# Kernel tuning notes

Hardware: AMD Instinct MI355X
Metric: run time of the kernel (lower is better)

Reference implementation:

```python
import jax, jax.numpy as jnp
import numpy as np

N, E, B = 50000, 600000, 64
ANN, D, STEPS, ETYPES, CLS = 64, 128, 5, 4, 10


def setup_inputs() -> dict:
    key = jax.random.key(0)
    ks = jax.random.split(key, 12)
    return {
        "annotation": jax.random.normal(ks[0], (N, ANN), jnp.float32),
        "src": jax.random.randint(ks[1], (E,), 0, N),
        "dst": jax.random.randint(ks[2], (E,), 0, N),
        "etypes": jax.random.randint(ks[3], (E,), 0, ETYPES),
        "node2graph": jnp.sort(jax.random.randint(ks[4], (N,), 0, B)),
        "labels": jax.random.randint(ks[5], (B,), 0, CLS),
        "W_lin": jax.random.normal(ks[6], (ETYPES, D, D), jnp.float32) / np.sqrt(D),
        "b_lin": jnp.zeros((ETYPES, D), jnp.float32),
        "W_ih": jax.random.normal(ks[7], (3 * D, D), jnp.float32) / np.sqrt(D),
        "W_hh": jax.random.normal(ks[8], (3 * D, D), jnp.float32) / np.sqrt(D),
        "b_ih": jnp.zeros((3 * D,), jnp.float32),
        "b_hh": jnp.zeros((3 * D,), jnp.float32),
        "gate_w": jax.random.normal(ks[9], (1, ANN + D), jnp.float32) / np.sqrt(ANN + D),
        "gate_b": jnp.zeros((1,), jnp.float32),
        "out_w": jax.random.normal(ks[10], (CLS, ANN + D), jnp.float32) / np.sqrt(ANN + D),
        "out_b": jnp.zeros((CLS,), jnp.float32),
    }


def reference(annotation, src, dst, etypes, node2graph, labels,
              W_lin, b_lin, W_ih, W_hh, b_ih, b_hh,
              gate_w, gate_b, out_w, out_b):
    n = annotation.shape[0]
    d = W_lin.shape[-1]
    nb = labels.shape[0]
    # h1 = [annotation | zeros]  -> [N, D]
    h = jnp.concatenate(
        [annotation, jnp.zeros((n, d - annotation.shape[1]), annotation.dtype)], -1)

    def step(hc, _):
        # per-edge-type linear transform of all nodes: [K, N, D]
        all_t = jnp.einsum('nd,kod->kno', hc, W_lin) + b_lin[:, None, :]
        m = all_t[etypes, src]                                  # [E, D] messages
        a = jax.ops.segment_sum(m, dst, num_segments=n)         # [N, D] aggregate
        # torch GRUCell: gates ordered (reset, update, new)
        gi = a @ W_ih.T + b_ih
        gh = hc @ W_hh.T + b_hh
        i_r, i_z, i_n = jnp.split(gi, 3, axis=-1)
        h_r, h_z, h_n = jnp.split(gh, 3, axis=-1)
        r = jax.nn.sigmoid(i_r + h_r)
        z = jax.nn.sigmoid(i_z + h_z)
        nt = jnp.tanh(i_n + r * h_n)
        return (1.0 - z) * nt + z * hc, None

    h, _ = jax.lax.scan(step, h, None, length=STEPS)
    feat = jnp.concatenate([h, annotation], -1)                 # [N, D+ANN]
    # global attention pooling: segment softmax over nodes per graph
    gate = (feat @ gate_w.T + gate_b)[:, 0]                     # [N]
    gmax = jax.ops.segment_max(gate, node2graph, num_segments=nb)
    ex = jnp.exp(gate - gmax[node2graph])
    denom = jax.ops.segment_sum(ex, node2graph, num_segments=nb)
    alpha = ex / denom[node2graph]
    readout = jax.ops.segment_sum(feat * alpha[:, None], node2graph, num_segments=nb)
    logits = readout @ out_w.T + out_b                          # [B, CLS]
    preds = jnp.argmax(logits, -1)
    logp = jax.nn.log_softmax(logits, -1)
    loss = -jnp.mean(jnp.take_along_axis(logp, labels[:, None], axis=1))
    return loss, preds
```

## Files before the change

### kernel.cpp

```cpp
#include <hip/hip_runtime.h>
#include <math.h>

#define DD 128
#define ANND 64
#define NSTEPS 5
#define NTYPES 4
#define NCLS 10

typedef __attribute__((ext_vector_type(8))) short short8v;
typedef __attribute__((ext_vector_type(4))) float f32x4;

__device__ __forceinline__ void split2(float x, unsigned short& hi, unsigned short& lo) {
  unsigned u = __float_as_uint(x);
  unsigned hb = (u + 0x7FFFu + ((u >> 16) & 1u)) >> 16;
  hi = (unsigned short)hb;
  float r = x - __uint_as_float(hb << 16);
  unsigned v = __float_as_uint(r);
  lo = (unsigned short)((v + 0x7FFFu + ((v >> 16) & 1u)) >> 16);
}

__device__ __forceinline__ float bf2f(unsigned short u) {
  return __uint_as_float(((unsigned)u) << 16);
}
__device__ __forceinline__ float rec2(const unsigned short* hi, const unsigned short* lo, size_t i) {
  return bf2f(hi[i]) + bf2f(lo[i]);
}
__device__ __forceinline__ float lo16f(unsigned u) { return __uint_as_float(u << 16); }
__device__ __forceinline__ float hi16f(unsigned u) { return __uint_as_float(u & 0xffff0000u); }

__device__ __forceinline__ void gload16(const unsigned short* g, unsigned short* l) {
  __builtin_amdgcn_global_load_lds(
      (const __attribute__((address_space(1))) unsigned int*)(const void*)g,
      (__attribute__((address_space(3))) unsigned int*)(void*)l, 16, 0, 0);
}

__global__ void k_init(const float* __restrict__ ann,
    unsigned short* __restrict__ hhi, unsigned short* __restrict__ hlo, int n, int npad) {
  int idx = blockIdx.x * blockDim.x + threadIdx.x;
  if (idx >= npad * DD) return;
  int node = idx >> 7, d = idx & 127;
  float v = (node < n && d < ANND) ? ann[node * ANND + d] : 0.0f;
  unsigned short hi, lo; split2(v, hi, lo);
  hhi[idx] = hi; hlo[idx] = lo;
}

__global__ void k_deg4(const int* __restrict__ dst, const int* __restrict__ et,
    int* __restrict__ deg4, int e) {
  int i = blockIdx.x * blockDim.x + threadIdx.x;
  if (i < e) atomicAdd(&deg4[dst[i] * 4 + et[i]], 1);
}

__global__ __launch_bounds__(1024) void k_scan(const int* __restrict__ deg4,
    int* __restrict__ base, int n) {
  __shared__ int part[1024];
  int t = threadIdx.x;
  int chunk = (n + 1023) >> 10;
  int s = t * chunk, e = min(n, s + chunk);
  int sum = 0;
  for (int i = s; i < e; ++i) {
    const int4 d4 = *(const int4*)(deg4 + (size_t)i * 4);
    sum += d4.x + d4.y + d4.z + d4.w;
  }
  part[t] = sum;
  __syncthreads();
  int own = sum;
  for (int off = 1; off < 1024; off <<= 1) {
    int v = (t >= off) ? part[t - off] : 0;
    __syncthreads();
    part[t] += v;
    __syncthreads();
  }
  int run = part[t] - own;
  for (int i = s; i < e; ++i) {
    base[i] = run;
    const int4 d4 = *(const int4*)(deg4 + (size_t)i * 4);
    run += d4.x + d4.y + d4.z + d4.w;
  }
  if (s < n && e == n) base[n] = run;
}

__global__ void k_place(const int* __restrict__ src, const int* __restrict__ dst,
    const int* __restrict__ et, const int* __restrict__ base, int* __restrict__ cursor,
    int* __restrict__ cpack, int e) {
  int i = blockIdx.x * blockDim.x + threadIdx.x;
  if (i >= e) return;
  int d = dst[i];
  int pos = base[d] + atomicAdd(&cursor[d], 1);
  cpack[pos] = src[i] | (et[i] << 18);
}

__global__ void k_aggh(const unsigned* __restrict__ hhiU, const unsigned* __restrict__ hloU,
    const int* __restrict__ base, const int* __restrict__ cpack,
    unsigned* __restrict__ A3hiU, unsigned* __restrict__ A3loU, int nbase, int cc) {
  int w = threadIdx.x >> 6;
  int lane = threadIdx.x & 63;
  int local = blockIdx.x * 4 + w;
  if (local >= cc) return;
  int node = nbase + local;
  int s = base[node], e = base[node + 1];
  float a0x = 0.f, a0y = 0.f, a1x = 0.f, a1y = 0.f;
  float a2x = 0.f, a2y = 0.f, a3x = 0.f, a3y = 0.f;
  for (int t0 = s; t0 < e; t0 += 64) {
    int cnt = min(64, e - t0);
    int mypk = (t0 + lane < e) ? cpack[t0 + lane] : 0;
    int i = 0;
    for (; i + 4 <= cnt; i += 4) {
      int pk0 = __shfl(mypk, i), pk1 = __shfl(mypk, i + 1);
      int pk2 = __shfl(mypk, i + 2), pk3 = __shfl(mypk, i + 3);
      unsigned uh0 = hhiU[(size_t)(pk0 & 0x3ffff) * 64 + lane];
      unsigned ul0 = hloU[(size_t)(pk0 & 0x3ffff) * 64 + lane];
      unsigned uh1 = hhiU[(size_t)(pk1 & 0x3ffff) * 64 + lane];
      unsigned ul1 = hloU[(size_t)(pk1 & 0x3ffff) * 64 + lane];
      unsigned uh2 = hhiU[(size_t)(pk2 & 0x3ffff) * 64 + lane];
      unsigned ul2 = hloU[(size_t)(pk2 & 0x3ffff) * 64 + lane];
      unsigned uh3 = hhiU[(size_t)(pk3 & 0x3ffff) * 64 + lane];
      unsigned ul3 = hloU[(size_t)(pk3 & 0x3ffff) * 64 + lane];
      float v0x = lo16f(uh0) + lo16f(ul0), v0y = hi16f(uh0) + hi16f(ul0);
      float v1x = lo16f(uh1) + lo16f(ul1), v1y = hi16f(uh1) + hi16f(ul1);
      float v2x = lo16f(uh2) + lo16f(ul2), v2y = hi16f(uh2) + hi16f(ul2);
      float v3x = lo16f(uh3) + lo16f(ul3), v3y = hi16f(uh3) + hi16f(ul3);
      int t;
      t = pk0 >> 18;
      if (t == 0) { a0x += v0x; a0y += v0y; } else if (t == 1) { a1x += v0x; a1y += v0y; }
      else if (t == 2) { a2x += v0x; a2y += v0y; } else { a3x += v0x; a3y += v0y; }
      t = pk1 >> 18;
      if (t == 0) { a0x += v1x; a0y += v1y; } else if (t == 1) { a1x += v1x; a1y += v1y; }
      else if (t == 2) { a2x += v1x; a2y += v1y; } else { a3x += v1x; a3y += v1y; }
      t = pk2 >> 18;
      if (t == 0) { a0x += v2x; a0y += v2y; } else if (t == 1) { a1x += v2x; a1y += v2y; }
      else if (t == 2) { a2x += v2x; a2y += v2y; } else { a3x += v2x; a3y += v2y; }
      t = pk3 >> 18;
      if (t == 0) { a0x += v3x; a0y += v3y; } else if (t == 1) { a1x += v3x; a1y += v3y; }
      else if (t == 2) { a2x += v3x; a2y += v3y; } else { a3x += v3x; a3y += v3y; }
    }
    for (; i < cnt; ++i) {
      int pk = __shfl(mypk, i);
      unsigned uh = hhiU[(size_t)(pk & 0x3ffff) * 64 + lane];
      unsigned ul = hloU[(size_t)(pk & 0x3ffff) * 64 + lane];
      float vx = lo16f(uh) + lo16f(ul), vy = hi16f(uh) + hi16f(ul);
      int t = pk >> 18;
      if (t == 0) { a0x += vx; a0y += vy; } else if (t == 1) { a1x += vx; a1y += vy; }
      else if (t == 2) { a2x += vx; a2y += vy; } else { a3x += vx; a3y += vy; }
    }
  }
  size_t bu = (size_t)local * 256 + lane;
  unsigned short h0, l0, h1, l1;
  split2(a0x, h0, l0); split2(a0y, h1, l1);
  A3hiU[bu] = (unsigned)h0 | ((unsigned)h1 << 16);
  A3loU[bu] = (unsigned)l0 | ((unsigned)l1 << 16);
  split2(a1x, h0, l0); split2(a1y, h1, l1);
  A3hiU[bu + 64] = (unsigned)h0 | ((unsigned)h1 << 16);
  A3loU[bu + 64] = (unsigned)l0 | ((unsigned)l1 << 16);
  split2(a2x, h0, l0); split2(a2y, h1, l1);
  A3hiU[bu + 128] = (unsigned)h0 | ((unsigned)h1 << 16);
  A3loU[bu + 128] = (unsigned)l0 | ((unsigned)l1 << 16);
  split2(a3x, h0, l0); split2(a3y, h1, l1);
  A3hiU[bu + 192] = (unsigned)h0 | ((unsigned)h1 << 16);
  A3loU[bu + 192] = (unsigned)l0 | ((unsigned)l1 << 16);
}

__global__ void k_fusew(const float* __restrict__ Wih, const float* __restrict__ Wlin,
    float* __restrict__ VW) {
  int idx = blockIdx.x * blockDim.x + threadIdx.x;
  if (idx >= 384 * 512) return;
  int c = idx >> 9, kd = idx & 511;
  int k = kd >> 7, d = kd & 127;
  const float* wi = Wih + (size_t)c * DD;
  const float* wl = Wlin + (size_t)k * DD * DD + d;
  float s = 0.f;
  for (int o = 0; o < DD; ++o) s += wi[o] * wl[(size_t)o * DD];
  VW[idx] = s;
}

__global__ void k_wbig(const float* __restrict__ VW, const float* __restrict__ Whh,
    unsigned short* __restrict__ WbH, unsigned short* __restrict__ WbL) {
  int idx = blockIdx.x * blockDim.x + threadIdx.x;
  if (idx >= 512 * 640) return;
  int c = idx / 640, k = idx % 640;
  float v;
  if (c < 256)      v = (k < 512) ? VW[(size_t)c * 512 + k] : Whh[(size_t)c * DD + (k - 512)];
  else if (c < 384) v = (k < 512) ? VW[(size_t)c * 512 + k] : 0.f;
  else              v = (k < 512) ? 0.f : Whh[(size_t)(c - 128) * DD + (k - 512)];
  int g = c >> 7, d = c & 127;
  int cn = ((d >> 5) << 7) + (((d >> 4) & 1) << 6) + (g << 4) + (d & 15);
  unsigned short h, l; split2(v, h, l);
  WbH[(size_t)cn * 640 + k] = h;
  WbL[(size_t)cn * 640 + k] = l;
}

__global__ void k_fuseb(const float* __restrict__ Wih, const float* __restrict__ bih,
    const float* __restrict__ bhh, const float* __restrict__ blin,
    float* __restrict__ bias_big, float* __restrict__ cb4) {
  int c = blockIdx.x * blockDim.x + threadIdx.x;
  if (c >= 512) return;
  float b;
  if (c < 256) b = bih[c] + bhh[c];
  else if (c < 384) b = bih[c];
  else b = bhh[c - 128];
  bias_big[c] = b;
  for (int k = 0; k < NTYPES; ++k) {
    float s = 0.f;
    if (c < 384) {
      const float* wi = Wih + (size_t)c * DD;
      const float* bl = blin + (size_t)k * DD;
      for (int o = 0; o < DD; ++o) s += wi[o] * bl[o];
    }
    cb4[k * 512 + c] = s;
  }
}

__global__ __launch_bounds__(256) void k_gru4(
    const unsigned short* __restrict__ A3hi, const unsigned short* __restrict__ A3lo,
    const unsigned short* __restrict__ Hhi, const unsigned short* __restrict__ Hlo,
    const unsigned short* __restrict__ WbH, const unsigned short* __restrict__ WbL,
    const float* __restrict__ bias_big, const float* __restrict__ cb4,
    const int* __restrict__ deg4,
    unsigned short* __restrict__ Ohi, unsigned short* __restrict__ Olo,
    int nbase, int cc) {
  __shared__ unsigned short lds[4 * 128 * 32];
  int tid = threadIdx.x;
  int wid = tid >> 6, lane = tid & 63;
  int wr = wid & 1, wc = wid >> 1;
  int lr = lane & 15, lk = lane >> 4;
  int rowbase = blockIdx.x * 128;
  int wtb = blockIdx.y * 128;
  f32x4 acc[4][4];
  #pragma unroll
  for (int mm = 0; mm < 4; ++mm)
    #pragma unroll
    for (int g = 0; g < 4; ++g) acc[mm][g] = (f32x4){0.f, 0.f, 0.f, 0.f};

  int srow = tid >> 2;
  int sc = (tid & 3) ^ (srow & 3);
  int wub = (tid & ~63) * 8;

  for (int k0 = 0; k0 < 640; k0 += 32) {
    __syncthreads();
    #pragma unroll
    for (int i = 0; i < 2; ++i) {
      int row = srow + i * 64;
      unsigned short* dst = (unsigned short*)lds + i * 2048 + wub;
      const unsigned short *xsH, *xsL;
      if (k0 < 512) {
        size_t off = (size_t)(rowbase + row) * 512 + k0 + sc * 8;
        xsH = A3hi + off; xsL = A3lo + off;
      } else {
        size_t off = (size_t)(nbase + rowbase + row) * DD + (k0 - 512) + sc * 8;
        xsH = Hhi + off; xsL = Hlo + off;
      }
      size_t woff = (size_t)(wtb + row) * 640 + k0 + sc * 8;
      gload16(xsH, dst);
      gload16(xsL, dst + 4096);
      gload16(WbH + woff, dst + 8192);
      gload16(WbL + woff, dst + 12288);
    }
    __syncthreads();

    int nnSkip = (k0 < 512) ? 3 : 2;
    short8v xh[4], xl[4];
    #pragma unroll
    for (int mm = 0; mm < 4; ++mm) {
      int row = wr * 64 + mm * 16 + lr;
      int a = row * 32 + ((lk ^ (row & 3)) << 3);
      xh[mm] = *(const short8v*)(lds + a);
      xl[mm] = *(const short8v*)(lds + 4096 + a);
    }
    #pragma unroll
    for (int nn = 0; nn < 4; ++nn) {
      if (nn == nnSkip) continue;
      int row = wc * 64 + nn * 16 + lr;
      int a = row * 32 + ((lk ^ (row & 3)) << 3);
      short8v wh = *(const short8v*)(lds + 8192 + a);
      short8v wl = *(const short8v*)(lds + 12288 + a);
      #pragma unroll
      for (int mm = 0; mm < 4; ++mm) {
        acc[mm][nn] = __builtin_amdgcn_mfma_f32_16x16x32_bf16(xh[mm], wh, acc[mm][nn], 0, 0, 0);
        acc[mm][nn] = __builtin_amdgcn_mfma_f32_16x16x32_bf16(xh[mm], wl, acc[mm][nn], 0, 0, 0);
        acc[mm][nn] = __builtin_amdgcn_mfma_f32_16x16x32_bf16(xl[mm], wh, acc[mm][nn], 0, 0, 0);
      }
    }
  }

  int d = blockIdx.y * 32 + wc * 16 + lr;
  float bsr = bias_big[d], bsz = bias_big[128 + d];
  float bgn = bias_big[256 + d], bhn = bias_big[384 + d];
  float cbr[4], cbz[4], cbn[4];
  #pragma unroll
  for (int k = 0; k < 4; ++k) {
    cbr[k] = cb4[k * 512 + d];
    cbz[k] = cb4[k * 512 + 128 + d];
    cbn[k] = cb4[k * 512 + 256 + d];
  }
  #pragma unroll
  for (int mm = 0; mm < 4; ++mm) {
    #pragma unroll
    for (int j = 0; j < 4; ++j) {
      int row = rowbase + wr * 64 + mm * 16 + lk * 4 + j;
      if (row < cc) {
        int4 dg = *(const int4*)(deg4 + (size_t)row * 4);
        float s_r = acc[mm][0][j] + bsr + dg.x * cbr[0] + dg.y * cbr[1] + dg.z * cbr[2] + dg.w * cbr[3];
        float s_z = acc[mm][1][j] + bsz + dg.x * cbz[0] + dg.y * cbz[1] + dg.z * cbz[2] + dg.w * cbz[3];
        float g_n = acc[mm][2][j] + bgn + dg.x * cbn[0] + dg.y * cbn[1] + dg.z * cbn[2] + dg.w * cbn[3];
        float h_n = acc[mm][3][j] + bhn;
        float r = 1.f / (1.f + expf(-s_r));
        float z = 1.f / (1.f + expf(-s_z));
        float nt = tanhf(g_n + r * h_n);
        size_t gidx = (size_t)(nbase + row) * DD + d;
        float hv = (1.f - z) * nt + z * rec2(Hhi, Hlo, gidx);
        unsigned short uh, ul; split2(hv, uh, ul);
        Ohi[gidx] = uh; Olo[gidx] = ul;
      }
    }
  }
}

__global__ void k_gate(const unsigned short* __restrict__ hhi,
    const unsigned short* __restrict__ hlo, const float* __restrict__ ann,
    const float* __restrict__ gw, const float* __restrict__ gb,
    float* __restrict__ gate, int n) {
  int gt = blockIdx.x * blockDim.x + threadIdx.x;
  int wv = gt >> 6;
  int lane = threadIdx.x & 63;
  if (wv >= n) return;
  float p = rec2(hhi, hlo, (size_t)wv * DD + lane) * gw[lane]
          + rec2(hhi, hlo, (size_t)wv * DD + 64 + lane) * gw[64 + lane]
          + ann[(size_t)wv * ANND + lane] * gw[128 + lane];
  for (int off = 32; off; off >>= 1) p += __shfl_down(p, off);
  if (lane == 0) gate[wv] = p + gb[0];
}

__global__ void k_bounds(const int* __restrict__ n2g, int* __restrict__ startg,
    int* __restrict__ endg, int n) {
  int i = blockIdx.x * blockDim.x + threadIdx.x;
  if (i >= n) return;
  int g = n2g[i];
  if (i == 0 || n2g[i - 1] != g) startg[g] = i;
  if (i == n - 1 || n2g[i + 1] != g) endg[g] = i + 1;
}

__global__ __launch_bounds__(256) void k_mden(const float* __restrict__ gate,
    const int* __restrict__ startg, const int* __restrict__ endg,
    float* __restrict__ mg, float* __restrict__ invg) {
  __shared__ float red[256];
  int g = blockIdx.x;
  int s = startg[g], e = endg[g];
  int tid = threadIdx.x;
  float m = -1e30f;
  for (int i = s + tid; i < e; i += 256) m = fmaxf(m, gate[i]);
  red[tid] = m; __syncthreads();
  for (int off = 128; off; off >>= 1) {
    if (tid < off) red[tid] = fmaxf(red[tid], red[tid + off]);
    __syncthreads();
  }
  m = red[0];
  __syncthreads();
  float sum = 0.f;
  for (int i = s + tid; i < e; i += 256) sum += expf(gate[i] - m);
  red[tid] = sum; __syncthreads();
  for (int off = 128; off; off >>= 1) {
    if (tid < off) red[tid] += red[tid + off];
    __syncthreads();
  }
  if (tid == 0) { mg[g] = m; invg[g] = (s < e) ? 1.f / red[0] : 0.f; }
}

__global__ __launch_bounds__(256) void k_pool2(const float* __restrict__ gate,
    const unsigned* __restrict__ hhiU, const unsigned* __restrict__ hloU,
    const float* __restrict__ ann, const int* __restrict__ startg,
    const int* __restrict__ endg, const float* __restrict__ mg,
    const float* __restrict__ invg, float* __restrict__ readout) {
  __shared__ float redx[256], redy[256];
  int g = blockIdx.x;
  int s = startg[g], e = endg[g];
  int nl = threadIdx.x >> 6, lane = threadIdx.x & 63;
  float m = mg[g], inv = invg[g];
  if (blockIdx.y == 0) {
    float ax = 0.f, ay = 0.f;
    for (int i = s + nl; i < e; i += 4) {
      float al = expf(gate[i] - m) * inv;
      unsigned uh = hhiU[(size_t)i * 64 + lane];
      unsigned ul = hloU[(size_t)i * 64 + lane];
      ax += al * (lo16f(uh) + lo16f(ul));
      ay += al * (hi16f(uh) + hi16f(ul));
    }
    redx[threadIdx.x] = ax; redy[threadIdx.x] = ay;
    __syncthreads();
    if (nl == 0) {
      float sx = redx[lane] + redx[64 + lane] + redx[128 + lane] + redx[192 + lane];
      float sy = redy[lane] + redy[64 + lane] + redy[128 + lane] + redy[192 + lane];
      readout[g * (DD + ANND) + 2 * lane] = sx;
      readout[g * (DD + ANND) + 2 * lane + 1] = sy;
    }
  } else {
    float acc = 0.f;
    for (int i = s + nl; i < e; i += 4) {
      float al = expf(gate[i] - m) * inv;
      acc += al * ann[(size_t)i * ANND + lane];
    }
    redx[threadIdx.x] = acc;
    __syncthreads();
    if (nl == 0)
      readout[g * (DD + ANND) + DD + lane] =
          redx[lane] + redx[64 + lane] + redx[128 + lane] + redx[192 + lane];
  }
}

__global__ void k_logits(const float* __restrict__ readout, const float* __restrict__ ow,
    const float* __restrict__ ob, const int* __restrict__ labels,
    float* __restrict__ out, int B) {
  __shared__ float lsum[64];
  int g = threadIdx.x;
  float loss_c = 0.f;
  if (g < B) {
    float lg[NCLS];
    float mx = -1e30f;
    int best = 0;
    for (int c = 0; c < NCLS; ++c) {
      float acc = ob[c];
      const float* r = readout + g * (DD + ANND);
      const float* w = ow + c * (DD + ANND);
      for (int d = 0; d < DD + ANND; ++d) acc += r[d] * w[d];
      lg[c] = acc;
      if (acc > mx) { mx = acc; best = c; }
    }
    float se = 0.f;
    for (int c = 0; c < NCLS; ++c) se += expf(lg[c] - mx);
    float lse = mx + logf(se);
    loss_c = -(lg[labels[g]] - lse);
    out[1 + g] = (float)best;
  }
  lsum[threadIdx.x] = loss_c;
  __syncthreads();
  for (int off = 32; off; off >>= 1) {
    if (threadIdx.x < off) lsum[threadIdx.x] += lsum[threadIdx.x + off];
    __syncthreads();
  }
  if (threadIdx.x == 0) out[0] = lsum[0] / (float)B;
}

extern "C" void kernel_launch(void* const* d_in, const int* in_sizes, int n_in,
                              void* d_out, int out_size, void* d_ws, size_t ws_size,
                              hipStream_t stream) {
  const float* annotation = (const float*)d_in[0];
  const int*   src        = (const int*)d_in[1];
  const int*   dst        = (const int*)d_in[2];
  const int*   et         = (const int*)d_in[3];
  const int*   n2g        = (const int*)d_in[4];
  const int*   labels     = (const int*)d_in[5];
  const float* W_lin      = (const float*)d_in[6];
  const float* b_lin      = (const float*)d_in[7];
  const float* W_ih       = (const float*)d_in[8];
  const float* W_hh       = (const float*)d_in[9];
  const float* b_ih       = (const float*)d_in[10];
  const float* b_hh       = (const float*)d_in[11];
  const float* gate_w     = (const float*)d_in[12];
  const float* gate_b     = (const float*)d_in[13];
  const float* out_w      = (const float*)d_in[14];
  const float* out_b      = (const float*)d_in[15];

  int N = in_sizes[0] / ANND;
  int E = in_sizes[1];
  int B = in_sizes[5];
  int Np = (N + 127) & ~127;

  auto rup = [](size_t b) { return (b + 255) & ~(size_t)255; };
  size_t fixed = 0;
  fixed += 4 * rup((size_t)Np * DD * 2);
  fixed += rup((size_t)N * 4);
  fixed += rup((size_t)B * (DD + ANND) * 4);
  fixed += 4 * rup((size_t)B * 4);
  fixed += rup((size_t)(N + 1) * 4);
  fixed += rup((size_t)N * 4);
  fixed += rup((size_t)N * 16);
  fixed += rup((size_t)E * 4);
  fixed += rup(384 * 512 * 4);
  fixed += 2 * rup(512 * 640 * 2);
  fixed += rup(512 * 4) + rup(4 * 512 * 4);
  size_t slack = 1 << 20;
  size_t avail = (ws_size > fixed + slack) ? ws_size - fixed - slack : 0;
  long long ch = (long long)(avail / 2048);
  int CH = (int)((ch / 128) * 128);
  if (CH < 128) CH = 128;
  if (CH > Np) CH = Np;

  char* wsP = (char*)d_ws;
  auto alloc = [&](size_t bytes) -> void* {
    void* p = (void*)wsP;
    wsP += (bytes + 255) & ~(size_t)255;
    return p;
  };
  unsigned short* hP_hi[2], *hP_lo[2];
  hP_hi[0] = (unsigned short*)alloc((size_t)Np * DD * 2);
  hP_lo[0] = (unsigned short*)alloc((size_t)Np * DD * 2);
  hP_hi[1] = (unsigned short*)alloc((size_t)Np * DD * 2);
  hP_lo[1] = (unsigned short*)alloc((size_t)Np * DD * 2);
  float* gate = (float*)alloc((size_t)N * 4);
  float* readout = (float*)alloc((size_t)B * (DD + ANND) * 4);
  int* startg = (int*)alloc((size_t)B * 4);
  int* endg   = (int*)alloc((size_t)B * 4);
  float* mg   = (float*)alloc((size_t)B * 4);
  float* invg = (float*)alloc((size_t)B * 4);
  int* base   = (int*)alloc((size_t)(N + 1) * 4);
  int* cursor = (int*)alloc((size_t)N * 4);
  int* deg4   = (int*)alloc((size_t)N * 16);
  int* cpack  = (int*)alloc((size_t)E * 4);
  float* VW   = (float*)alloc(384 * 512 * 4);
  unsigned short* WbH = (unsigned short*)alloc(512 * 640 * 2);
  unsigned short* WbL = (unsigned short*)alloc(512 * 640 * 2);
  float* bias_big = (float*)alloc(512 * 4);
  float* cb4  = (float*)alloc(4 * 512 * 4);
  unsigned short* A3hi = (unsigned short*)alloc((size_t)CH * 512 * 2);
  unsigned short* A3lo = (unsigned short*)alloc((size_t)CH * 512 * 2);

  k_init<<<(Np * DD + 255) / 256, 256, 0, stream>>>(annotation, hP_hi[0], hP_lo[0], N, Np);
  hipMemsetAsync(cursor, 0, (size_t)N * 4, stream);
  hipMemsetAsync(deg4, 0, (size_t)N * 16, stream);
  hipMemsetAsync(startg, 0x7f, (size_t)B * 4, stream);
  hipMemsetAsync(endg, 0, (size_t)B * 4, stream);
  k_deg4<<<(E + 255) / 256, 256, 0, stream>>>(dst, et, deg4, E);
  k_scan<<<1, 1024, 0, stream>>>(deg4, base, N);
  k_place<<<(E + 255) / 256, 256, 0, stream>>>(src, dst, et, base, cursor, cpack, E);
  k_bounds<<<(N + 255) / 256, 256, 0, stream>>>(n2g, startg, endg, N);
  k_fusew<<<(384 * 512 + 255) / 256, 256, 0, stream>>>(W_ih, W_lin, VW);
  k_wbig<<<(512 * 640 + 255) / 256, 256, 0, stream>>>(VW, W_hh, WbH, WbL);
  k_fuseb<<<2, 256, 0, stream>>>(W_ih, b_ih, b_hh, b_lin, bias_big, cb4);

  int cur = 0;
  for (int s = 0; s < NSTEPS; ++s) {
    int nxt = cur ^ 1;
    for (int nbase = 0; nbase < N; nbase += CH) {
      int cc = min(CH, N - nbase);
      int cgrid = (cc + 127) / 128;
      k_aggh<<<(cc + 3) / 4, 256, 0, stream>>>(
          (const unsigned*)hP_hi[cur], (const unsigned*)hP_lo[cur], base, cpack,
          (unsigned*)A3hi, (unsigned*)A3lo, nbase, cc);
      k_gru4<<<dim3(cgrid, 4), 256, 0, stream>>>(A3hi, A3lo,
          hP_hi[cur], hP_lo[cur], WbH, WbL, bias_big, cb4,
          deg4 + (size_t)nbase * 4, hP_hi[nxt], hP_lo[nxt], nbase, cc);
    }
    cur ^= 1;
  }

  k_gate<<<(N * 64 + 255) / 256, 256, 0, stream>>>(
      hP_hi[cur], hP_lo[cur], annotation, gate_w, gate_b, gate, N);
  k_mden<<<B, 256, 0, stream>>>(gate, startg, endg, mg, invg);
  k_pool2<<<dim3(B, 2), 256, 0, stream>>>(gate, (const unsigned*)hP_hi[cur],
      (const unsigned*)hP_lo[cur], annotation, startg, endg, mg, invg, readout);
  k_logits<<<1, 64, 0, stream>>>(readout, out_w, out_b, labels, (float*)d_out, B);
}
```

Measured before the change: 1.240 ms.

## Retile GRU GEMM to 64-row node tiles with 256-column weight tiles

The fused GRU GEMM kernel changes from 128 nodes by 128 gate-columns per block (four column blocks) to 64 nodes by 256 gate-columns (two column blocks). Each wave now owns 64 output columns across all node rows, and the grid is reordered so column tiles vary fastest. This cuts how many times the X operand (aggregated messages and hidden state) is reread from global memory, and consecutive blocks share the same node rows. In exchange each block loads twice as much weight data per k-step, and the LDS layout changes.

```diff
diff --git a/kernel.cpp b/kernel.cpp
--- a/kernel.cpp
+++ b/kernel.cpp
@@ -209,7 +209,7 @@
   }
 }
 
-__global__ __launch_bounds__(256) void k_gru4(
+__global__ __launch_bounds__(256) void k_gru5(
     const unsigned short* __restrict__ A3hi, const unsigned short* __restrict__ A3lo,
     const unsigned short* __restrict__ Hhi, const unsigned short* __restrict__ Hlo,
     const unsigned short* __restrict__ WbH, const unsigned short* __restrict__ WbL,
@@ -217,42 +217,46 @@
     const int* __restrict__ deg4,
     unsigned short* __restrict__ Ohi, unsigned short* __restrict__ Olo,
     int nbase, int cc) {
-  __shared__ unsigned short lds[4 * 128 * 32];
+  __shared__ unsigned short ldsX[2 * 64 * 32];
+  __shared__ unsigned short ldsW[2 * 256 * 32];
   int tid = threadIdx.x;
-  int wid = tid >> 6, lane = tid & 63;
-  int wr = wid & 1, wc = wid >> 1;
+  int wc = tid >> 6, lane = tid & 63;
   int lr = lane & 15, lk = lane >> 4;
-  int rowbase = blockIdx.x * 128;
-  int wtb = blockIdx.y * 128;
+  int rowbase = blockIdx.y * 64;
+  int ytile = blockIdx.x;
+  int wtb = ytile * 256;
   f32x4 acc[4][4];
   #pragma unroll
   for (int mm = 0; mm < 4; ++mm)
     #pragma unroll
     for (int g = 0; g < 4; ++g) acc[mm][g] = (f32x4){0.f, 0.f, 0.f, 0.f};
 
-  int srow = tid >> 2;
-  int sc = (tid & 3) ^ (srow & 3);
-  int wub = (tid & ~63) * 8;
+  int srow = tid >> 2, sc0 = tid & 3;
+  int xcs = sc0 ^ (srow & 3);
+  unsigned short* xdst = ldsX + (tid & ~63) * 8;
 
   for (int k0 = 0; k0 < 640; k0 += 32) {
     __syncthreads();
-    #pragma unroll
-    for (int i = 0; i < 2; ++i) {
-      int row = srow + i * 64;
-      unsigned short* dst = (unsigned short*)lds + i * 2048 + wub;
+    {
       const unsigned short *xsH, *xsL;
       if (k0 < 512) {
-        size_t off = (size_t)(rowbase + row) * 512 + k0 + sc * 8;
+        size_t off = (size_t)(rowbase + srow) * 512 + k0 + xcs * 8;
         xsH = A3hi + off; xsL = A3lo + off;
       } else {
-        size_t off = (size_t)(nbase + rowbase + row) * DD + (k0 - 512) + sc * 8;
+        size_t off = (size_t)(nbase + rowbase + srow) * DD + (k0 - 512) + xcs * 8;
         xsH = Hhi + off; xsL = Hlo + off;
       }
-      size_t woff = (size_t)(wtb + row) * 640 + k0 + sc * 8;
-      gload16(xsH, dst);
-      gload16(xsL, dst + 4096);
-      gload16(WbH + woff, dst + 8192);
-      gload16(WbL + woff, dst + 12288);
+      gload16(xsH, xdst);
+      gload16(xsL, xdst + 2048);
+    }
+    #pragma unroll
+    for (int i = 0; i < 4; ++i) {
+      int wrow = i * 64 + srow;
+      int wcs = sc0 ^ (wrow & 3);
+      size_t woff = (size_t)(wtb + wrow) * 640 + k0 + wcs * 8;
+      unsigned short* wdst = ldsW + i * 2048 + (tid & ~63) * 8;
+      gload16(WbH + woff, wdst);
+      gload16(WbL + woff, wdst + 8192);
     }
     __syncthreads();
 
@@ -260,18 +264,18 @@
     short8v xh[4], xl[4];
     #pragma unroll
     for (int mm = 0; mm < 4; ++mm) {
-      int row = wr * 64 + mm * 16 + lr;
-      int a = row * 32 + ((lk ^ (row & 3)) << 3);
-      xh[mm] = *(const short8v*)(lds + a);
-      xl[mm] = *(const short8v*)(lds + 4096 + a);
+      int r = mm * 16 + lr;
+      int a = r * 32 + ((lk ^ (r & 3)) << 3);
+      xh[mm] = *(const short8v*)(ldsX + a);
+      xl[mm] = *(const short8v*)(ldsX + 2048 + a);
     }
     #pragma unroll
     for (int nn = 0; nn < 4; ++nn) {
       if (nn == nnSkip) continue;
-      int row = wc * 64 + nn * 16 + lr;
-      int a = row * 32 + ((lk ^ (row & 3)) << 3);
-      short8v wh = *(const short8v*)(lds + 8192 + a);
-      short8v wl = *(const short8v*)(lds + 12288 + a);
+      int rw = wc * 64 + nn * 16 + lr;
+      int a = rw * 32 + ((lk ^ (rw & 3)) << 3);
+      short8v wh = *(const short8v*)(ldsW + a);
+      short8v wl = *(const short8v*)(ldsW + 8192 + a);
       #pragma unroll
       for (int mm = 0; mm < 4; ++mm) {
         acc[mm][nn] = __builtin_amdgcn_mfma_f32_16x16x32_bf16(xh[mm], wh, acc[mm][nn], 0, 0, 0);
@@ -281,7 +285,7 @@
     }
   }
 
-  int d = blockIdx.y * 32 + wc * 16 + lr;
+  int d = ytile * 64 + wc * 16 + lr;
   float bsr = bias_big[d], bsz = bias_big[128 + d];
   float bgn = bias_big[256 + d], bhn = bias_big[384 + d];
   float cbr[4], cbz[4], cbn[4];
@@ -295,7 +299,7 @@
   for (int mm = 0; mm < 4; ++mm) {
     #pragma unroll
     for (int j = 0; j < 4; ++j) {
-      int row = rowbase + wr * 64 + mm * 16 + lk * 4 + j;
+      int row = rowbase + mm * 16 + lk * 4 + j;
       if (row < cc) {
         int4 dg = *(const int4*)(deg4 + (size_t)row * 4);
         float s_r = acc[mm][0][j] + bsr + dg.x * cbr[0] + dg.y * cbr[1] + dg.z * cbr[2] + dg.w * cbr[3];
@@ -530,11 +534,11 @@
     int nxt = cur ^ 1;
     for (int nbase = 0; nbase < N; nbase += CH) {
       int cc = min(CH, N - nbase);
-      int cgrid = (cc + 127) / 128;
+      int cgrid = (cc + 63) / 64;
       k_aggh<<<(cc + 3) / 4, 256, 0, stream>>>(
           (const unsigned*)hP_hi[cur], (const unsigned*)hP_lo[cur], base, cpack,
           (unsigned*)A3hi, (unsigned*)A3lo, nbase, cc);
-      k_gru4<<<dim3(cgrid, 4), 256, 0, stream>>>(A3hi, A3lo,
+      k_gru5<<<dim3(2, cgrid), 256, 0, stream>>>(A3hi, A3lo,
           hP_hi[cur], hP_lo[cur], WbH, WbL, bias_big, cb4,
           deg4 + (size_t)nbase * 4, hP_hi[nxt], hP_lo[nxt], nbase, cc);
     }
```

After: 1.235 ms. About the same (-0.4%).
